# Kernel tuning notes

Measured on AMD Instinct MI355X. Metric: run time of the kernel, lower is better.

Reference implementation:

```python
import jax, jax.numpy as jnp
import numpy as np

DILATION_RATE = 4
SEGMENT_SIZE = 512


def setup_inputs() -> dict:
    key = jax.random.key(0)
    x = jax.random.normal(key, (4, 8192, 1024), dtype=jnp.float32)
    return {"x": x}


def reference(x):
    """LongNet-style dilated attention.

    For each offset in range(dilation_rate): take the strided slice
    x[:, offset::r, :], split it into segments of length `segment_size`,
    run full softmax(q k^T / sqrt(d)) v attention inside each segment
    (q=k=v=the slice; attention dim is the full d_model, matching how the
    original feeds [B, n_seg, seg, d_model] to FlashAttention), scatter the
    result back to the strided positions, and average the dilation heads
    (softmax over uniform logits == 1/r weights).

    Since seq_len % (r * segment_size) == 0, the r strided slices tile the
    sequence exactly, so we vectorize over offsets with a single reshape:
    position p = i*r + offset  ->  xr[:, i, offset, :].
    """
    r, seg = DILATION_RATE, SEGMENT_SIZE
    B, S, D = x.shape
    n = S // r            # tokens per strided slice
    g = n // seg          # segments per slice
    scale = 1.0 / jnp.sqrt(jnp.asarray(D, dtype=x.dtype))

    xs = x.reshape(B, g, seg, r, D)  # [B, g, seg, r, D]; axis r = dilation offset
    # segment-local attention, independently per (batch, offset, segment)
    scores = jnp.einsum("bgqrd,bgkrd->brgqk", xs, xs) * scale  # [B, r, g, seg, seg]
    probs = jax.nn.softmax(scores, axis=-1)
    out = jnp.einsum("brgqk,bgkrd->bgqrd", probs, xs)          # [B, g, seg, r, D]
    # scatter back to strided positions (pure reshape, since slices tile S),
    # then weighted sum with uniform softmax weights == divide by r.
    return out.reshape(B, S, D) / r
```

## Files before the change

kernel.cpp:

```cpp
#include <hip/hip_runtime.h>
#include <stdint.h>

typedef __bf16 bf16x8  __attribute__((ext_vector_type(8)));
typedef float  f32x4   __attribute__((ext_vector_type(4)));

#define LOG2E    1.44269504088896340736f
#define SM_SCALE 0.03125f

typedef __attribute__((address_space(1))) const uint32_t gau32;
typedef __attribute__((address_space(3))) uint32_t       lau32;
#define GLD16(g, l) __builtin_amdgcn_global_load_lds((gau32*)(g), (lau32*)(l), 16, 0, 0)

__device__ __forceinline__ uint32_t f2bf(float f) {
  uint32_t u = __builtin_bit_cast(uint32_t, f);
  u += 0x7FFFu + ((u >> 16) & 1u);
  return u >> 16;
}
__device__ __forceinline__ uint32_t pk2(float a, float b) {
  return f2bf(a) | (f2bf(b) << 16);
}
__device__ __forceinline__ uint4 pack8(float4 a, float4 b) {
  uint4 r;
  r.x = pk2(a.x, a.y); r.y = pk2(a.z, a.w);
  r.z = pk2(b.x, b.y); r.w = pk2(b.z, b.w);
  return r;
}

__global__ __launch_bounds__(256)
void prep_comb(const float* __restrict__ x, uint16_t* __restrict__ vt,
               uint16_t* __restrict__ xs) {
  __shared__ char tl[64 * 144];
  const int t    = threadIdx.x;
  const int blk  = blockIdx.x;
  const int dc   = blk & 15;
  const int kb   = (blk >> 4) & 7;
  const int prob = blk >> 7;
  const int b  = prob >> 4, off = (prob >> 2) & 3, gs = prob & 3;

  const int key = t >> 2, dq = t & 3;
  const float* src = x + ((size_t)(b * 8192 + gs * 2048 + (kb * 64 + key) * 4 + off)) * 1024
                     + dc * 64 + dq * 16;
  float4 f0 = *(const float4*)(src);
  float4 f1 = *(const float4*)(src + 4);
  float4 f2 = *(const float4*)(src + 8);
  float4 f3 = *(const float4*)(src + 12);
  const int swz = (key & 7) << 4;
  *(uint4*)(tl + key * 144 + ((dq * 32) ^ swz))      = pack8(f0, f1);
  *(uint4*)(tl + key * 144 + ((dq * 32 + 16) ^ swz)) = pack8(f2, f3);
  __syncthreads();
  {
    const int d = t >> 2, kq = t & 3;
    uint32_t w[8];
#pragma unroll
    for (int i = 0; i < 8; ++i) {
      int k0 = kq * 16 + 2 * i, k1 = k0 + 1;
      uint32_t a  = *(const uint16_t*)(tl + k0 * 144 + ((2 * d) ^ ((k0 & 7) << 4)));
      uint32_t bb = *(const uint16_t*)(tl + k1 * 144 + ((2 * d) ^ ((k1 & 7) << 4)));
      w[i] = a | (bb << 16);
    }
    uint16_t* dst = vt + ((size_t)(prob * 1024 + dc * 64 + d)) * 512 + kb * 64 + kq * 16;
    *(uint4*)(dst)     = *(uint4*)&w[0];
    *(uint4*)(dst + 8) = *(uint4*)&w[4];
  }
  {
    const int row = t >> 2, j = t & 3;
    uint4 w0 = *(const uint4*)(tl + row * 144 + j * 32);
    uint4 w1 = *(const uint4*)(tl + row * 144 + j * 32 + 16);
    char* dst = (char*)xs +
        ((size_t)((prob * 512 + kb * 64 + row) * 16 + dc)) * 128 + j * 32;
    *(uint4*)(dst)      = w0;
    *(uint4*)(dst + 16) = w1;
  }
}

#define B3_STRIDE 73728
#define B3_QOFF   65536
#define R3_0      65536
#define R3_1      67584
#define LDS3_BYTES 147456

__global__ __launch_bounds__(512, 2)
void dilattn3(const uint16_t* __restrict__ xs, const uint16_t* __restrict__ vt,
              float* __restrict__ out) {
  extern __shared__ char smem[];

  const int tid  = threadIdx.x;
  const int lane = tid & 63;
  const int wid  = tid >> 6;
  const int h    = lane >> 4;
  const int l15  = lane & 15;
  const int psw  = (l15 & 7) << 4;

  const int blk  = blockIdx.x;
  const int prob = ((blk & 7) << 3) | (blk >> 6);
  const int q0   = ((blk >> 3) & 7) * 64;
  const int b    = prob >> 4;
  const int off  = (prob >> 2) & 3;
  const int gs   = prob & 3;

  const char* xp = (const char*)xs + (size_t)prob * 1048576;

  const int r8 = lane >> 3, g8 = lane & 7;
  const char* gK = xp + (size_t)(wid * 8 + r8) * 2048 + g8 * 16;
  const char* gQ = xp + (size_t)(q0 + wid * 8 + r8) * 2048 + g8 * 16;

  const int akR = (64 * wid + l15) * 128;
  const int bqR = B3_QOFF + l15 * 128;
  const int fb0 = (16 * h) ^ psw;

  f32x4 S[4][4];
#pragma unroll
  for (int i = 0; i < 4; ++i)
#pragma unroll
    for (int j = 0; j < 4; ++j) S[i][j] = (f32x4){0.f, 0.f, 0.f, 0.f};

  {
    {
      char* base = smem;
#pragma unroll
      for (int ii = 0; ii < 8; ++ii)
        GLD16(gK + ii * 131072, base + wid * 1024 + ii * 8192);
      GLD16(gQ, base + B3_QOFF + wid * 1024);
    }
    __syncthreads();
#pragma unroll 1
    for (int dc = 0; dc < 16; ++dc) {
      if (dc < 15) {
        char* nb = smem + ((dc + 1) & 1) * B3_STRIDE;
        const int go = (dc + 1) * 128;
#pragma unroll
        for (int ii = 0; ii < 8; ++ii)
          GLD16(gK + ii * 131072 + go, nb + wid * 1024 + ii * 8192);
        GLD16(gQ + go, nb + B3_QOFF + wid * 1024);
      }
      const char* base = smem + (dc & 1) * B3_STRIDE;
#pragma unroll
      for (int s = 0; s < 2; ++s) {
        const int fb = fb0 ^ (s << 6);
        bf16x8 aK[4], bq[4];
#pragma unroll
        for (int kt = 0; kt < 4; ++kt)
          aK[kt] = *(const bf16x8*)(base + akR + kt * 2048 + fb);
#pragma unroll
        for (int qt = 0; qt < 4; ++qt)
          bq[qt] = *(const bf16x8*)(base + bqR + qt * 2048 + fb);
#pragma unroll
        for (int kt = 0; kt < 4; ++kt)
#pragma unroll
          for (int qt = 0; qt < 4; ++qt)
            S[kt][qt] = __builtin_amdgcn_mfma_f32_16x16x32_bf16(aK[kt], bq[qt], S[kt][qt], 0, 0, 0);
      }
      __syncthreads();
    }
  }

  float mq[4], sq[4], rinv[4];
#pragma unroll
  for (int qt = 0; qt < 4; ++qt) {
    float m = S[0][qt][0];
#pragma unroll
    for (int kt = 0; kt < 4; ++kt)
#pragma unroll
      for (int r = 0; r < 4; ++r) m = fmaxf(m, S[kt][qt][r]);
    m = fmaxf(m, __shfl_xor(m, 16, 64));
    m = fmaxf(m, __shfl_xor(m, 32, 64));
    mq[qt] = m;
  }
  if (h == 0) {
#pragma unroll
    for (int qt = 0; qt < 4; ++qt)
      *(float*)(smem + R3_0 + (wid * 64 + 16 * qt + l15) * 4) = mq[qt];
  }
  __syncthreads();
#pragma unroll
  for (int qt = 0; qt < 4; ++qt) {
    float m = -3e38f;
#pragma unroll
    for (int w = 0; w < 8; ++w)
      m = fmaxf(m, *(const float*)(smem + R3_0 + (w * 64 + 16 * qt + l15) * 4));
    mq[qt] = m * SM_SCALE;
    sq[qt] = 0.f;
  }
#pragma unroll
  for (int kt = 0; kt < 4; ++kt)
#pragma unroll
    for (int qt = 0; qt < 4; ++qt)
#pragma unroll
      for (int r = 0; r < 4; ++r) {
        float v = exp2f((S[kt][qt][r] * SM_SCALE - mq[qt]) * LOG2E);
        S[kt][qt][r] = v;
        sq[qt] += v;
      }
#pragma unroll
  for (int qt = 0; qt < 4; ++qt) {
    sq[qt] += __shfl_xor(sq[qt], 16, 64);
    sq[qt] += __shfl_xor(sq[qt], 32, 64);
  }
  if (h == 0) {
#pragma unroll
    for (int qt = 0; qt < 4; ++qt)
      *(float*)(smem + R3_1 + (wid * 64 + 16 * qt + l15) * 4) = sq[qt];
  }
  __syncthreads();
#pragma unroll
  for (int qt = 0; qt < 4; ++qt) {
    float l = 0.f;
#pragma unroll
    for (int w = 0; w < 8; ++w)
      l += *(const float*)(smem + R3_1 + (w * 64 + 16 * qt + l15) * 4);
    rinv[qt] = 0.25f / l;
  }
#pragma unroll
  for (int kt = 0; kt < 4; ++kt)
#pragma unroll
    for (int qt = 0; qt < 4; ++qt) {
      uint2 w2;
      w2.x = pk2(S[kt][qt][0] * rinv[qt], S[kt][qt][1] * rinv[qt]);
      w2.y = pk2(S[kt][qt][2] * rinv[qt], S[kt][qt][3] * rinv[qt]);
      *(uint2*)(smem + (16 * qt + l15) * 1024 +
                ((128 * wid + 32 * kt + 8 * h) ^ psw)) = w2;
    }
  __syncthreads();

  f32x4 acc[8][4];
#pragma unroll
  for (int i = 0; i < 8; ++i)
#pragma unroll
    for (int j = 0; j < 4; ++j) acc[i][j] = (f32x4){0.f, 0.f, 0.f, 0.f};

  const char* vtW = (const char*)(vt + ((size_t)(prob * 1024 + 128 * wid + l15)) * 512 + 8 * h);
  bf16x8 vcur[8], vnxt[8];
#pragma unroll
  for (int cd = 0; cd < 8; ++cd)
    vcur[cd] = *(const bf16x8*)(vtW + ((cd >> 2) * 64 + (cd & 3) * 16) * 1024);
#pragma unroll 1
  for (int ks = 0; ks < 16; ++ks) {
    if (ks < 15) {
#pragma unroll
      for (int cd = 0; cd < 8; ++cd)
        vnxt[cd] = *(const bf16x8*)(vtW + ((cd >> 2) * 64 + (cd & 3) * 16) * 1024 + (ks + 1) * 64);
    }
    bf16x8 pa[4];
#pragma unroll
    for (int qt = 0; qt < 4; ++qt)
      pa[qt] = *(const bf16x8*)(smem + (16 * qt + l15) * 1024 + ((64 * ks + 16 * h) ^ psw));
#pragma unroll
    for (int cd = 0; cd < 8; ++cd)
#pragma unroll
      for (int qt = 0; qt < 4; ++qt)
        acc[cd][qt] = __builtin_amdgcn_mfma_f32_16x16x32_bf16(pa[qt], vcur[cd], acc[cd][qt], 0, 0, 0);
#pragma unroll
    for (int cd = 0; cd < 8; ++cd) vcur[cd] = vnxt[cd];
  }

#pragma unroll
  for (int cd = 0; cd < 8; ++cd) {
    const int d = 128 * wid + (cd >> 2) * 64 + (cd & 3) * 16 + l15;
#pragma unroll
    for (int qt = 0; qt < 4; ++qt)
#pragma unroll
      for (int r = 0; r < 4; ++r) {
        const int qq = q0 + 16 * qt + 4 * h + r;
        out[((size_t)(b * 8192 + gs * 2048 + qq * 4 + off)) * 1024 + d] = acc[cd][qt][r];
      }
  }
}

#define KP_OFF 0
#define Q_OFF  65536
#define RED0   65536
#define RED1   67584
#define LDS_BYTES 73728

__global__ __launch_bounds__(256)
void vt_prepass(const float* __restrict__ x, uint16_t* __restrict__ vt) {
  __shared__ char tl[64 * 144];
  const int t    = threadIdx.x;
  const int blk  = blockIdx.x;
  const int dc   = blk & 15;
  const int kb   = (blk >> 4) & 7;
  const int prob = blk >> 7;
  const int b  = prob >> 4, off = (prob >> 2) & 3, gs = prob & 3;

  const int key = t >> 2, dq = t & 3;
  const float* src = x + ((size_t)(b * 8192 + gs * 2048 + (kb * 64 + key) * 4 + off)) * 1024
                     + dc * 64 + dq * 16;
  float4 f0 = *(const float4*)(src);
  float4 f1 = *(const float4*)(src + 4);
  float4 f2 = *(const float4*)(src + 8);
  float4 f3 = *(const float4*)(src + 12);
  const int swz = (key & 7) << 4;
  *(uint4*)(tl + key * 144 + ((dq * 32) ^ swz))      = pack8(f0, f1);
  *(uint4*)(tl + key * 144 + ((dq * 32 + 16) ^ swz)) = pack8(f2, f3);
  __syncthreads();
  const int d = t >> 2, kq = t & 3;
  uint32_t w[8];
#pragma unroll
  for (int i = 0; i < 8; ++i) {
    int k0 = kq * 16 + 2 * i, k1 = k0 + 1;
    uint32_t a  = *(const uint16_t*)(tl + k0 * 144 + ((2 * d) ^ ((k0 & 7) << 4)));
    uint32_t bb = *(const uint16_t*)(tl + k1 * 144 + ((2 * d) ^ ((k1 & 7) << 4)));
    w[i] = a | (bb << 16);
  }
  uint16_t* dst = vt + ((size_t)(prob * 1024 + dc * 64 + d)) * 512 + kb * 64 + kq * 16;
  *(uint4*)(dst)     = *(uint4*)&w[0];
  *(uint4*)(dst + 8) = *(uint4*)&w[4];
}

template <int USE_VT>
__global__ __launch_bounds__(512, 2)
void dilattn2(const float* __restrict__ x, const uint16_t* __restrict__ vt,
              float* __restrict__ out) {
  extern __shared__ char smem[];

  const int tid  = threadIdx.x;
  const int lane = tid & 63;
  const int wid  = tid >> 6;
  const int h    = lane >> 4;
  const int l15  = lane & 15;
  const int psw  = (l15 & 7) << 4;

  const int blk  = blockIdx.x;
  const int prob = blk >> 3;
  const int q0   = (blk & 7) * 64;
  const int b    = prob >> 4;
  const int off  = (prob >> 2) & 3;
  const int gs   = prob & 3;

  const float* xb = x + (size_t)b * (8192u * 1024u);

  const int srow = tid >> 3;
  const int sg   = tid & 7;
  const float* gK = xb + (size_t)(gs * 2048 + srow * 4 + off) * 1024 + sg * 8;
  const float* gQ = xb + (size_t)(gs * 2048 + (q0 + srow) * 4 + off) * 1024 + sg * 8;
  const int kWr = srow * 128 + ((sg * 16) ^ ((srow & 7) << 4));
  const int qWr = Q_OFF + kWr;

  const int akR = (64 * wid + l15) * 128;
  const int bqR = Q_OFF + l15 * 128;
  const int fb0 = (16 * h) ^ psw;

  f32x4 S[4][4];
#pragma unroll
  for (int i = 0; i < 4; ++i)
#pragma unroll
    for (int j = 0; j < 4; ++j) S[i][j] = (f32x4){0.f, 0.f, 0.f, 0.f};

  float4 kp[16], qp[2];
#pragma unroll
  for (int j = 0; j < 8; ++j) {
    const float* p = gK + (size_t)j * 262144;
    kp[2 * j]     = *(const float4*)(p);
    kp[2 * j + 1] = *(const float4*)(p + 4);
  }
  qp[0] = *(const float4*)(gQ);
  qp[1] = *(const float4*)(gQ + 4);

#pragma unroll 1
  for (int dc = 0; dc < 16; ++dc) {
#pragma unroll
    for (int j = 0; j < 8; ++j)
      *(uint4*)(smem + KP_OFF + kWr + j * 8192) = pack8(kp[2 * j], kp[2 * j + 1]);
    *(uint4*)(smem + qWr) = pack8(qp[0], qp[1]);
    if (dc < 15) {
      const int doff = (dc + 1) * 64;
#pragma unroll
      for (int j = 0; j < 8; ++j) {
        const float* p = gK + (size_t)j * 262144 + doff;
        kp[2 * j]     = *(const float4*)(p);
        kp[2 * j + 1] = *(const float4*)(p + 4);
      }
      qp[0] = *(const float4*)(gQ + doff);
      qp[1] = *(const float4*)(gQ + doff + 4);
    }
    __syncthreads();
#pragma unroll
    for (int s = 0; s < 2; ++s) {
      const int fb = fb0 ^ (s << 6);
      bf16x8 aK[4], bq[4];
#pragma unroll
      for (int kt = 0; kt < 4; ++kt)
        aK[kt] = *(const bf16x8*)(smem + akR + kt * 2048 + fb);
#pragma unroll
      for (int qt = 0; qt < 4; ++qt)
        bq[qt] = *(const bf16x8*)(smem + bqR + qt * 2048 + fb);
#pragma unroll
      for (int kt = 0; kt < 4; ++kt)
#pragma unroll
        for (int qt = 0; qt < 4; ++qt)
          S[kt][qt] = __builtin_amdgcn_mfma_f32_16x16x32_bf16(aK[kt], bq[qt], S[kt][qt], 0, 0, 0);
    }
    __syncthreads();
  }

  float mq[4], sq[4], rinv[4];
#pragma unroll
  for (int qt = 0; qt < 4; ++qt) {
    float m = S[0][qt][0];
#pragma unroll
    for (int kt = 0; kt < 4; ++kt)
#pragma unroll
      for (int r = 0; r < 4; ++r) m = fmaxf(m, S[kt][qt][r]);
    m = fmaxf(m, __shfl_xor(m, 16, 64));
    m = fmaxf(m, __shfl_xor(m, 32, 64));
    mq[qt] = m;
  }
  if (h == 0) {
#pragma unroll
    for (int qt = 0; qt < 4; ++qt)
      *(float*)(smem + RED0 + (wid * 64 + 16 * qt + l15) * 4) = mq[qt];
  }
  __syncthreads();
#pragma unroll
  for (int qt = 0; qt < 4; ++qt) {
    float m = -3e38f;
#pragma unroll
    for (int w = 0; w < 8; ++w)
      m = fmaxf(m, *(const float*)(smem + RED0 + (w * 64 + 16 * qt + l15) * 4));
    mq[qt] = m * SM_SCALE;
    sq[qt] = 0.f;
  }
#pragma unroll
  for (int kt = 0; kt < 4; ++kt)
#pragma unroll
    for (int qt = 0; qt < 4; ++qt)
#pragma unroll
      for (int r = 0; r < 4; ++r) {
        float v = exp2f((S[kt][qt][r] * SM_SCALE - mq[qt]) * LOG2E);
        S[kt][qt][r] = v;
        sq[qt] += v;
      }
#pragma unroll
  for (int qt = 0; qt < 4; ++qt) {
    sq[qt] += __shfl_xor(sq[qt], 16, 64);
    sq[qt] += __shfl_xor(sq[qt], 32, 64);
  }
  if (h == 0) {
#pragma unroll
    for (int qt = 0; qt < 4; ++qt)
      *(float*)(smem + RED1 + (wid * 64 + 16 * qt + l15) * 4) = sq[qt];
  }
  __syncthreads();
#pragma unroll
  for (int qt = 0; qt < 4; ++qt) {
    float l = 0.f;
#pragma unroll
    for (int w = 0; w < 8; ++w)
      l += *(const float*)(smem + RED1 + (w * 64 + 16 * qt + l15) * 4);
    rinv[qt] = 0.25f / l;
  }
#pragma unroll
  for (int kt = 0; kt < 4; ++kt)
#pragma unroll
    for (int qt = 0; qt < 4; ++qt) {
      uint2 w2;
      w2.x = pk2(S[kt][qt][0] * rinv[qt], S[kt][qt][1] * rinv[qt]);
      w2.y = pk2(S[kt][qt][2] * rinv[qt], S[kt][qt][3] * rinv[qt]);
      *(uint2*)(smem + KP_OFF + (16 * qt + l15) * 1024 +
                ((128 * wid + 32 * kt + 8 * h) ^ psw)) = w2;
    }
  __syncthreads();

  f32x4 acc[8][4];
#pragma unroll
  for (int i = 0; i < 8; ++i)
#pragma unroll
    for (int j = 0; j < 4; ++j) acc[i][j] = (f32x4){0.f, 0.f, 0.f, 0.f};

  const uint16_t* vtW = nullptr;
  if constexpr (USE_VT)
    vtW = vt + ((size_t)(prob * 1024 + 128 * wid + l15)) * 512 + 8 * h;

#pragma unroll 1
  for (int ks = 0; ks < 16; ++ks) {
    bf16x8 pa[4];
#pragma unroll
    for (int qt = 0; qt < 4; ++qt)
      pa[qt] = *(const bf16x8*)(smem + KP_OFF + (16 * qt + l15) * 1024 +
                                ((64 * ks + 16 * h) ^ psw));
#pragma unroll
    for (int cd = 0; cd < 8; ++cd) {
      bf16x8 v;
      if constexpr (USE_VT) {
        v = *(const bf16x8*)(vtW + (size_t)((cd >> 2) * 64 + (cd & 3) * 16) * 512 + 32 * ks);
      } else {
        const int d = 128 * wid + (cd >> 2) * 64 + (cd & 3) * 16 + l15;
        union { bf16x8 v; uint16_t u[8]; } a0;
#pragma unroll
        for (int jj = 0; jj < 8; ++jj) {
          int key = 32 * ks + 8 * h + jj;
          a0.u[jj] = (uint16_t)f2bf(xb[(size_t)(gs * 2048 + key * 4 + off) * 1024 + d]);
        }
        v = a0.v;
      }
#pragma unroll
      for (int qt = 0; qt < 4; ++qt)
        acc[cd][qt] = __builtin_amdgcn_mfma_f32_16x16x32_bf16(pa[qt], v, acc[cd][qt], 0, 0, 0);
    }
  }

#pragma unroll
  for (int cd = 0; cd < 8; ++cd) {
    const int d = 128 * wid + (cd >> 2) * 64 + (cd & 3) * 16 + l15;
#pragma unroll
    for (int qt = 0; qt < 4; ++qt)
#pragma unroll
      for (int r = 0; r < 4; ++r) {
        const int qq = q0 + 16 * qt + 4 * h + r;
        out[((size_t)(b * 8192 + gs * 2048 + qq * 4 + off)) * 1024 + d] = acc[cd][qt][r];
      }
  }
}

extern "C" void kernel_launch(void* const* d_in, const int* in_sizes, int n_in,
                              void* d_out, int out_size, void* d_ws, size_t ws_size,
                              hipStream_t stream) {
  const float* x = (const float*)d_in[0];
  float* out = (float*)d_out;
  (void)in_sizes; (void)n_in; (void)out_size;
  const size_t vt_bytes = 64ull * 1024 * 512 * 2;
  const size_t xs_bytes = 64ull * 512 * 16 * 128;
  if (ws_size >= vt_bytes + xs_bytes) {
    uint16_t* vtp = (uint16_t*)d_ws;
    uint16_t* xsp = (uint16_t*)((char*)d_ws + vt_bytes);
    hipFuncSetAttribute(reinterpret_cast<const void*>(dilattn3),
                        hipFuncAttributeMaxDynamicSharedMemorySize, LDS3_BYTES);
    prep_comb<<<8192, 256, 0, stream>>>(x, vtp, xsp);
    dilattn3<<<512, 512, LDS3_BYTES, stream>>>(xsp, vtp, out);
  } else if (ws_size >= vt_bytes) {
    uint16_t* vtp = (uint16_t*)d_ws;
    hipFuncSetAttribute(reinterpret_cast<const void*>(dilattn2<1>),
                        hipFuncAttributeMaxDynamicSharedMemorySize, LDS_BYTES);
    vt_prepass<<<8192, 256, 0, stream>>>(x, vtp);
    dilattn2<1><<<512, 512, LDS_BYTES, stream>>>(x, vtp, out);
  } else {
    hipFuncSetAttribute(reinterpret_cast<const void*>(dilattn2<0>),
                        hipFuncAttributeMaxDynamicSharedMemorySize, LDS_BYTES);
    dilattn2<0><<<512, 512, LDS_BYTES, stream>>>(x, nullptr, out);
  }
}
```

Before: 190.7 us.

## Restructure QK and PV loops with single barrier, prefetch V early, setprio MFMA

The QK^T loop now uses one barrier per iteration that waits only on vmcnt, so the global-to-LDS load for the next chunk is issued after that barrier instead of with a second sync. All LDS fragments are loaded before a prioritized MFMA burst. The first two V chunks are prefetched before the softmax phase, and the PV loop uses two ping-pong V register buffers so each load has a full MFMA block to hide its latency. Softmax barriers wait only on lgkmcnt. These changes raise register pressure and tighten the synchronization correctness margins.

```diff
diff --git a/kernel.cpp b/kernel.cpp
--- a/kernel.cpp
+++ b/kernel.cpp
@@ -10,6 +10,9 @@
 typedef __attribute__((address_space(1))) const uint32_t gau32;
 typedef __attribute__((address_space(3))) uint32_t       lau32;
 #define GLD16(g, l) __builtin_amdgcn_global_load_lds((gau32*)(g), (lau32*)(l), 16, 0, 0)
+
+#define LGKM_BAR() do { asm volatile("s_waitcnt lgkmcnt(0)" ::: "memory"); \
+  __builtin_amdgcn_s_barrier(); asm volatile("" ::: "memory"); } while (0)
 
 __device__ __forceinline__ uint32_t f2bf(float f) {
   uint32_t u = __builtin_bit_cast(uint32_t, f);
@@ -115,43 +118,55 @@
     for (int j = 0; j < 4; ++j) S[i][j] = (f32x4){0.f, 0.f, 0.f, 0.f};
 
   {
-    {
-      char* base = smem;
+    char* base0 = smem;
+#pragma unroll
+    for (int ii = 0; ii < 8; ++ii)
+      GLD16(gK + ii * 131072, base0 + wid * 1024 + ii * 8192);
+    GLD16(gQ, base0 + B3_QOFF + wid * 1024);
+  }
+#pragma unroll 1
+  for (int dc = 0; dc < 16; ++dc) {
+    asm volatile("s_waitcnt vmcnt(0)" ::: "memory");
+    __builtin_amdgcn_s_barrier();
+    asm volatile("" ::: "memory");
+    if (dc < 15) {
+      char* nb = smem + ((dc + 1) & 1) * B3_STRIDE;
+      const int go = (dc + 1) * 128;
 #pragma unroll
       for (int ii = 0; ii < 8; ++ii)
-        GLD16(gK + ii * 131072, base + wid * 1024 + ii * 8192);
-      GLD16(gQ, base + B3_QOFF + wid * 1024);
-    }
-    __syncthreads();
-#pragma unroll 1
-    for (int dc = 0; dc < 16; ++dc) {
-      if (dc < 15) {
-        char* nb = smem + ((dc + 1) & 1) * B3_STRIDE;
-        const int go = (dc + 1) * 128;
-#pragma unroll
-        for (int ii = 0; ii < 8; ++ii)
-          GLD16(gK + ii * 131072 + go, nb + wid * 1024 + ii * 8192);
-        GLD16(gQ + go, nb + B3_QOFF + wid * 1024);
-      }
-      const char* base = smem + (dc & 1) * B3_STRIDE;
-#pragma unroll
-      for (int s = 0; s < 2; ++s) {
-        const int fb = fb0 ^ (s << 6);
-        bf16x8 aK[4], bq[4];
-#pragma unroll
-        for (int kt = 0; kt < 4; ++kt)
-          aK[kt] = *(const bf16x8*)(base + akR + kt * 2048 + fb);
+        GLD16(gK + ii * 131072 + go, nb + wid * 1024 + ii * 8192);
+      GLD16(gQ + go, nb + B3_QOFF + wid * 1024);
+    }
+    const char* base = smem + (dc & 1) * B3_STRIDE;
+    bf16x8 aK[8], bq[8];
+#pragma unroll
+    for (int s = 0; s < 2; ++s) {
+      const int fb = fb0 ^ (s << 6);
+#pragma unroll
+      for (int kt = 0; kt < 4; ++kt)
+        aK[s * 4 + kt] = *(const bf16x8*)(base + akR + kt * 2048 + fb);
+#pragma unroll
+      for (int qt = 0; qt < 4; ++qt)
+        bq[s * 4 + qt] = *(const bf16x8*)(base + bqR + qt * 2048 + fb);
+    }
+    __builtin_amdgcn_s_setprio(1);
+#pragma unroll
+    for (int s = 0; s < 2; ++s)
+#pragma unroll
+      for (int kt = 0; kt < 4; ++kt)
 #pragma unroll
         for (int qt = 0; qt < 4; ++qt)
-          bq[qt] = *(const bf16x8*)(base + bqR + qt * 2048 + fb);
-#pragma unroll
-        for (int kt = 0; kt < 4; ++kt)
-#pragma unroll
-          for (int qt = 0; qt < 4; ++qt)
-            S[kt][qt] = __builtin_amdgcn_mfma_f32_16x16x32_bf16(aK[kt], bq[qt], S[kt][qt], 0, 0, 0);
-      }
-      __syncthreads();
-    }
+          S[kt][qt] = __builtin_amdgcn_mfma_f32_16x16x32_bf16(aK[s * 4 + kt], bq[s * 4 + qt],
+                                                              S[kt][qt], 0, 0, 0);
+    __builtin_amdgcn_s_setprio(0);
+  }
+
+  const char* vtW = (const char*)(vt + ((size_t)(prob * 1024 + 128 * wid + l15)) * 512 + 8 * h);
+  bf16x8 vA[8], vB[8];
+#pragma unroll
+  for (int cd = 0; cd < 8; ++cd) {
+    vA[cd] = *(const bf16x8*)(vtW + ((cd >> 2) * 64 + (cd & 3) * 16) * 1024);
+    vB[cd] = *(const bf16x8*)(vtW + ((cd >> 2) * 64 + (cd & 3) * 16) * 1024 + 64);
   }
 
   float mq[4], sq[4], rinv[4];
@@ -171,7 +186,7 @@
     for (int qt = 0; qt < 4; ++qt)
       *(float*)(smem + R3_0 + (wid * 64 + 16 * qt + l15) * 4) = mq[qt];
   }
-  __syncthreads();
+  LGKM_BAR();
 #pragma unroll
   for (int qt = 0; qt < 4; ++qt) {
     float m = -3e38f;
@@ -201,7 +216,7 @@
     for (int qt = 0; qt < 4; ++qt)
       *(float*)(smem + R3_1 + (wid * 64 + 16 * qt + l15) * 4) = sq[qt];
   }
-  __syncthreads();
+  LGKM_BAR();
 #pragma unroll
   for (int qt = 0; qt < 4; ++qt) {
     float l = 0.f;
@@ -220,7 +235,7 @@
       *(uint2*)(smem + (16 * qt + l15) * 1024 +
                 ((128 * wid + 32 * kt + 8 * h) ^ psw)) = w2;
     }
-  __syncthreads();
+  LGKM_BAR();
 
   f32x4 acc[8][4];
 #pragma unroll
@@ -228,29 +243,44 @@
 #pragma unroll
     for (int j = 0; j < 4; ++j) acc[i][j] = (f32x4){0.f, 0.f, 0.f, 0.f};
 
-  const char* vtW = (const char*)(vt + ((size_t)(prob * 1024 + 128 * wid + l15)) * 512 + 8 * h);
-  bf16x8 vcur[8], vnxt[8];
-#pragma unroll
-  for (int cd = 0; cd < 8; ++cd)
-    vcur[cd] = *(const bf16x8*)(vtW + ((cd >> 2) * 64 + (cd & 3) * 16) * 1024);
 #pragma unroll 1
-  for (int ks = 0; ks < 16; ++ks) {
-    if (ks < 15) {
+  for (int ks = 0; ks < 16; ks += 2) {
+    {
+      bf16x8 pa[4];
+#pragma unroll
+      for (int qt = 0; qt < 4; ++qt)
+        pa[qt] = *(const bf16x8*)(smem + (16 * qt + l15) * 1024 + ((64 * ks + 16 * h) ^ psw));
+      __builtin_amdgcn_s_setprio(1);
 #pragma unroll
       for (int cd = 0; cd < 8; ++cd)
-        vnxt[cd] = *(const bf16x8*)(vtW + ((cd >> 2) * 64 + (cd & 3) * 16) * 1024 + (ks + 1) * 64);
-    }
-    bf16x8 pa[4];
-#pragma unroll
-    for (int qt = 0; qt < 4; ++qt)
-      pa[qt] = *(const bf16x8*)(smem + (16 * qt + l15) * 1024 + ((64 * ks + 16 * h) ^ psw));
-#pragma unroll
-    for (int cd = 0; cd < 8; ++cd)
+#pragma unroll
+        for (int qt = 0; qt < 4; ++qt)
+          acc[cd][qt] = __builtin_amdgcn_mfma_f32_16x16x32_bf16(pa[qt], vA[cd], acc[cd][qt], 0, 0, 0);
+      __builtin_amdgcn_s_setprio(0);
+      if (ks + 2 < 16) {
+#pragma unroll
+        for (int cd = 0; cd < 8; ++cd)
+          vA[cd] = *(const bf16x8*)(vtW + ((cd >> 2) * 64 + (cd & 3) * 16) * 1024 + (ks + 2) * 64);
+      }
+    }
+    {
+      bf16x8 pa[4];
 #pragma unroll
       for (int qt = 0; qt < 4; ++qt)
-        acc[cd][qt] = __builtin_amdgcn_mfma_f32_16x16x32_bf16(pa[qt], vcur[cd], acc[cd][qt], 0, 0, 0);
-#pragma unroll
-    for (int cd = 0; cd < 8; ++cd) vcur[cd] = vnxt[cd];
+        pa[qt] = *(const bf16x8*)(smem + (16 * qt + l15) * 1024 + ((64 * (ks + 1) + 16 * h) ^ psw));
+      __builtin_amdgcn_s_setprio(1);
+#pragma unroll
+      for (int cd = 0; cd < 8; ++cd)
+#pragma unroll
+        for (int qt = 0; qt < 4; ++qt)
+          acc[cd][qt] = __builtin_amdgcn_mfma_f32_16x16x32_bf16(pa[qt], vB[cd], acc[cd][qt], 0, 0, 0);
+      __builtin_amdgcn_s_setprio(0);
+      if (ks + 3 < 16) {
+#pragma unroll
+        for (int cd = 0; cd < 8; ++cd)
+          vB[cd] = *(const bf16x8*)(vtW + ((cd >> 2) * 64 + (cd & 3) * 16) * 1024 + (ks + 3) * 64);
+      }
+    }
   }
 
 #pragma unroll
```

Result: faster. 182.7 us (-4.2%).

## Store X in MFMA fragment layout and stream K fragments directly from global

Applied to the files above, without the earlier changes.

The prep kernel now writes X in a per-16-row fragment-ordered layout so each lane loads its MFMA operand with a single contiguous 16-byte read. The attention kernel doubles to 16 waves (1024 threads), stages the full Q tile (all 1024 dims) in LDS once and reads K fragments straight from global into registers, which removes the double-buffered per-chunk LDS pipeline and its barriers. The PV stage also splits across 16 waves with fewer accumulators per wave. The trade-off is larger LDS use with a single block per CU, more cross-wave softmax reduction work, and no explicit prefetch of V.

```diff
diff --git a/kernel.cpp b/kernel.cpp
--- a/kernel.cpp
+++ b/kernel.cpp
@@ -28,7 +28,7 @@
 
 __global__ __launch_bounds__(256)
 void prep_comb(const float* __restrict__ x, uint16_t* __restrict__ vt,
-               uint16_t* __restrict__ xs) {
+               uint16_t* __restrict__ xf) {
   __shared__ char tl[64 * 144];
   const int t    = threadIdx.x;
   const int blk  = blockIdx.x;
@@ -63,24 +63,48 @@
     *(uint4*)(dst + 8) = *(uint4*)&w[4];
   }
   {
-    const int row = t >> 2, j = t & 3;
-    uint4 w0 = *(const uint4*)(tl + row * 144 + j * 32);
-    uint4 w1 = *(const uint4*)(tl + row * 144 + j * 32 + 16);
-    char* dst = (char*)xs +
-        ((size_t)((prob * 512 + kb * 64 + row) * 16 + dc)) * 128 + j * 32;
-    *(uint4*)(dst)      = w0;
-    *(uint4*)(dst + 16) = w1;
-  }
-}
-
-#define B3_STRIDE 73728
-#define B3_QOFF   65536
-#define R3_0      65536
-#define R3_1      67584
-#define LDS3_BYTES 147456
-
-__global__ __launch_bounds__(512, 2)
-void dilattn3(const uint16_t* __restrict__ xs, const uint16_t* __restrict__ vt,
+    const int row = t >> 2, p = t & 3;
+    const int dcl = p >> 1;
+    const int dq8b = (p & 1) * 2;
+    const int swz2 = (row & 7) << 4;
+    char* fbase = (char*)xf +
+        (((size_t)(prob * 32 + kb * 4 + (row >> 4)) * 32) + (dc * 2 + dcl)) * 1024;
+#pragma unroll
+    for (int i = 0; i < 2; ++i) {
+      const int dq8 = dq8b + i;
+      uint4 w = *(const uint4*)(tl + row * 144 + ((dcl * 64 + dq8 * 16) ^ swz2));
+      *(uint4*)(fbase + ((row & 15) + 16 * dq8) * 16) = w;
+    }
+  }
+}
+
+#define R4_0 131072
+#define R4_1 135168
+#define LDS4_BYTES 139264
+
+#define QKT_BODY(dc, A0, A1)                                                   \
+  {                                                                            \
+    const char* qb = smem + ((dc) >> 4) * 65536 + ((dc) & 15) * 4096 + lane16; \
+    bf16x8 b0 = *(const bf16x8*)(qb);                                          \
+    bf16x8 b1 = *(const bf16x8*)(qb + 1024);                                   \
+    bf16x8 b2 = *(const bf16x8*)(qb + 2048);                                   \
+    bf16x8 b3 = *(const bf16x8*)(qb + 3072);                                   \
+    S[0][0] = __builtin_amdgcn_mfma_f32_16x16x32_bf16(A0, b0, S[0][0], 0, 0, 0); \
+    S[0][1] = __builtin_amdgcn_mfma_f32_16x16x32_bf16(A0, b1, S[0][1], 0, 0, 0); \
+    S[0][2] = __builtin_amdgcn_mfma_f32_16x16x32_bf16(A0, b2, S[0][2], 0, 0, 0); \
+    S[0][3] = __builtin_amdgcn_mfma_f32_16x16x32_bf16(A0, b3, S[0][3], 0, 0, 0); \
+    S[1][0] = __builtin_amdgcn_mfma_f32_16x16x32_bf16(A1, b0, S[1][0], 0, 0, 0); \
+    S[1][1] = __builtin_amdgcn_mfma_f32_16x16x32_bf16(A1, b1, S[1][1], 0, 0, 0); \
+    S[1][2] = __builtin_amdgcn_mfma_f32_16x16x32_bf16(A1, b2, S[1][2], 0, 0, 0); \
+    S[1][3] = __builtin_amdgcn_mfma_f32_16x16x32_bf16(A1, b3, S[1][3], 0, 0, 0); \
+  }
+
+#define LOADA(dc, A0, A1) do {                       \
+    A0 = *(const bf16x8*)(xfA0 + (dc) * 1024);       \
+    A1 = *(const bf16x8*)(xfA1 + (dc) * 1024); } while (0)
+
+__global__ __launch_bounds__(1024, 4)
+void dilattn4(const char* __restrict__ xf, const char* __restrict__ vt,
               float* __restrict__ out) {
   extern __shared__ char smem[];
 
@@ -90,6 +114,7 @@
   const int h    = lane >> 4;
   const int l15  = lane & 15;
   const int psw  = (l15 & 7) << 4;
+  const int lane16 = lane * 16;
 
   const int blk  = blockIdx.x;
   const int prob = ((blk & 7) << 3) | (blk >> 6);
@@ -98,60 +123,39 @@
   const int off  = (prob >> 2) & 3;
   const int gs   = prob & 3;
 
-  const char* xp = (const char*)xs + (size_t)prob * 1048576;
-
-  const int r8 = lane >> 3, g8 = lane & 7;
-  const char* gK = xp + (size_t)(wid * 8 + r8) * 2048 + g8 * 16;
-  const char* gQ = xp + (size_t)(q0 + wid * 8 + r8) * 2048 + g8 * 16;
-
-  const int akR = (64 * wid + l15) * 128;
-  const int bqR = B3_QOFF + l15 * 128;
-  const int fb0 = (16 * h) ^ psw;
-
-  f32x4 S[4][4];
-#pragma unroll
-  for (int i = 0; i < 4; ++i)
+  const char* xfp = xf + (size_t)prob * 1048576;
+  const int qtile0 = q0 >> 4;
+
+#pragma unroll
+  for (int half = 0; half < 2; ++half)
+#pragma unroll
+    for (int i = 0; i < 4; ++i) {
+      const int c = wid * 4 + i;
+      const int dcl = c >> 2, qt = c & 3;
+      const char* src = xfp + ((size_t)(qtile0 + qt) * 32 + (half * 16 + dcl)) * 1024 + lane16;
+      GLD16(src, smem + half * 65536 + dcl * 4096 + qt * 1024);
+    }
+
+  const char* xfA0 = xfp + (size_t)(2 * wid) * 32768 + lane16;
+  const char* xfA1 = xfA0 + 32768;
+
+  f32x4 S[2][4];
+#pragma unroll
+  for (int i = 0; i < 2; ++i)
 #pragma unroll
     for (int j = 0; j < 4; ++j) S[i][j] = (f32x4){0.f, 0.f, 0.f, 0.f};
 
-  {
-    {
-      char* base = smem;
-#pragma unroll
-      for (int ii = 0; ii < 8; ++ii)
-        GLD16(gK + ii * 131072, base + wid * 1024 + ii * 8192);
-      GLD16(gQ, base + B3_QOFF + wid * 1024);
-    }
-    __syncthreads();
-#pragma unroll 1
-    for (int dc = 0; dc < 16; ++dc) {
-      if (dc < 15) {
-        char* nb = smem + ((dc + 1) & 1) * B3_STRIDE;
-        const int go = (dc + 1) * 128;
-#pragma unroll
-        for (int ii = 0; ii < 8; ++ii)
-          GLD16(gK + ii * 131072 + go, nb + wid * 1024 + ii * 8192);
-        GLD16(gQ + go, nb + B3_QOFF + wid * 1024);
-      }
-      const char* base = smem + (dc & 1) * B3_STRIDE;
-#pragma unroll
-      for (int s = 0; s < 2; ++s) {
-        const int fb = fb0 ^ (s << 6);
-        bf16x8 aK[4], bq[4];
-#pragma unroll
-        for (int kt = 0; kt < 4; ++kt)
-          aK[kt] = *(const bf16x8*)(base + akR + kt * 2048 + fb);
-#pragma unroll
-        for (int qt = 0; qt < 4; ++qt)
-          bq[qt] = *(const bf16x8*)(base + bqR + qt * 2048 + fb);
-#pragma unroll
-        for (int kt = 0; kt < 4; ++kt)
-#pragma unroll
-          for (int qt = 0; qt < 4; ++qt)
-            S[kt][qt] = __builtin_amdgcn_mfma_f32_16x16x32_bf16(aK[kt], bq[qt], S[kt][qt], 0, 0, 0);
-      }
-      __syncthreads();
-    }
+  bf16x8 aP0, aP1, aQ0, aQ1;
+  LOADA(0, aP0, aP1);
+  LOADA(1, aQ0, aQ1);
+  __syncthreads();
+
+#pragma unroll
+  for (int dc2 = 0; dc2 < 32; dc2 += 2) {
+    QKT_BODY(dc2, aP0, aP1);
+    if (dc2 + 2 < 32) LOADA(dc2 + 2, aP0, aP1);
+    QKT_BODY(dc2 + 1, aQ0, aQ1);
+    if (dc2 + 3 < 32) LOADA(dc2 + 3, aQ0, aQ1);
   }
 
   float mq[4], sq[4], rinv[4];
@@ -159,7 +163,7 @@
   for (int qt = 0; qt < 4; ++qt) {
     float m = S[0][qt][0];
 #pragma unroll
-    for (int kt = 0; kt < 4; ++kt)
+    for (int kt = 0; kt < 2; ++kt)
 #pragma unroll
       for (int r = 0; r < 4; ++r) m = fmaxf(m, S[kt][qt][r]);
     m = fmaxf(m, __shfl_xor(m, 16, 64));
@@ -169,20 +173,20 @@
   if (h == 0) {
 #pragma unroll
     for (int qt = 0; qt < 4; ++qt)
-      *(float*)(smem + R3_0 + (wid * 64 + 16 * qt + l15) * 4) = mq[qt];
+      *(float*)(smem + R4_0 + (wid * 64 + 16 * qt + l15) * 4) = mq[qt];
   }
   __syncthreads();
 #pragma unroll
   for (int qt = 0; qt < 4; ++qt) {
     float m = -3e38f;
 #pragma unroll
-    for (int w = 0; w < 8; ++w)
-      m = fmaxf(m, *(const float*)(smem + R3_0 + (w * 64 + 16 * qt + l15) * 4));
+    for (int w = 0; w < 16; ++w)
+      m = fmaxf(m, *(const float*)(smem + R4_0 + (w * 64 + 16 * qt + l15) * 4));
     mq[qt] = m * SM_SCALE;
     sq[qt] = 0.f;
   }
 #pragma unroll
-  for (int kt = 0; kt < 4; ++kt)
+  for (int kt = 0; kt < 2; ++kt)
 #pragma unroll
     for (int qt = 0; qt < 4; ++qt)
 #pragma unroll
@@ -199,71 +203,66 @@
   if (h == 0) {
 #pragma unroll
     for (int qt = 0; qt < 4; ++qt)
-      *(float*)(smem + R3_1 + (wid * 64 + 16 * qt + l15) * 4) = sq[qt];
+      *(float*)(smem + R4_1 + (wid * 64 + 16 * qt + l15) * 4) = sq[qt];
   }
   __syncthreads();
 #pragma unroll
   for (int qt = 0; qt < 4; ++qt) {
     float l = 0.f;
 #pragma unroll
-    for (int w = 0; w < 8; ++w)
-      l += *(const float*)(smem + R3_1 + (w * 64 + 16 * qt + l15) * 4);
+    for (int w = 0; w < 16; ++w)
+      l += *(const float*)(smem + R4_1 + (w * 64 + 16 * qt + l15) * 4);
     rinv[qt] = 0.25f / l;
   }
 #pragma unroll
-  for (int kt = 0; kt < 4; ++kt)
+  for (int kt = 0; kt < 2; ++kt)
 #pragma unroll
     for (int qt = 0; qt < 4; ++qt) {
       uint2 w2;
       w2.x = pk2(S[kt][qt][0] * rinv[qt], S[kt][qt][1] * rinv[qt]);
       w2.y = pk2(S[kt][qt][2] * rinv[qt], S[kt][qt][3] * rinv[qt]);
       *(uint2*)(smem + (16 * qt + l15) * 1024 +
-                ((128 * wid + 32 * kt + 8 * h) ^ psw)) = w2;
-    }
-  __syncthreads();
-
-  f32x4 acc[8][4];
-#pragma unroll
-  for (int i = 0; i < 8; ++i)
+                ((64 * wid + 32 * kt + 8 * h) ^ psw)) = w2;
+    }
+  __syncthreads();
+
+  f32x4 acc[4][4];
+#pragma unroll
+  for (int i = 0; i < 4; ++i)
 #pragma unroll
     for (int j = 0; j < 4; ++j) acc[i][j] = (f32x4){0.f, 0.f, 0.f, 0.f};
 
-  const char* vtW = (const char*)(vt + ((size_t)(prob * 1024 + 128 * wid + l15)) * 512 + 8 * h);
-  bf16x8 vcur[8], vnxt[8];
-#pragma unroll
-  for (int cd = 0; cd < 8; ++cd)
-    vcur[cd] = *(const bf16x8*)(vtW + ((cd >> 2) * 64 + (cd & 3) * 16) * 1024);
-#pragma unroll 1
+  const char* vtW = vt + (size_t)prob * 1048576 + (size_t)(64 * wid + l15) * 1024 + 16 * h;
+  const char* paB = smem + l15 * 1024;
+
+#pragma unroll 2
   for (int ks = 0; ks < 16; ++ks) {
-    if (ks < 15) {
-#pragma unroll
-      for (int cd = 0; cd < 8; ++cd)
-        vnxt[cd] = *(const bf16x8*)(vtW + ((cd >> 2) * 64 + (cd & 3) * 16) * 1024 + (ks + 1) * 64);
-    }
+    bf16x8 v0 = *(const bf16x8*)(vtW + 0 * 16384 + ks * 64);
+    bf16x8 v1 = *(const bf16x8*)(vtW + 1 * 16384 + ks * 64);
+    bf16x8 v2 = *(const bf16x8*)(vtW + 2 * 16384 + ks * 64);
+    bf16x8 v3 = *(const bf16x8*)(vtW + 3 * 16384 + ks * 64);
     bf16x8 pa[4];
 #pragma unroll
     for (int qt = 0; qt < 4; ++qt)
-      pa[qt] = *(const bf16x8*)(smem + (16 * qt + l15) * 1024 + ((64 * ks + 16 * h) ^ psw));
-#pragma unroll
-    for (int cd = 0; cd < 8; ++cd)
-#pragma unroll
-      for (int qt = 0; qt < 4; ++qt)
-        acc[cd][qt] = __builtin_amdgcn_mfma_f32_16x16x32_bf16(pa[qt], vcur[cd], acc[cd][qt], 0, 0, 0);
-#pragma unroll
-    for (int cd = 0; cd < 8; ++cd) vcur[cd] = vnxt[cd];
-  }
-
-#pragma unroll
-  for (int cd = 0; cd < 8; ++cd) {
-    const int d = 128 * wid + (cd >> 2) * 64 + (cd & 3) * 16 + l15;
-#pragma unroll
-    for (int qt = 0; qt < 4; ++qt)
-#pragma unroll
-      for (int r = 0; r < 4; ++r) {
-        const int qq = q0 + 16 * qt + 4 * h + r;
-        out[((size_t)(b * 8192 + gs * 2048 + qq * 4 + off)) * 1024 + d] = acc[cd][qt][r];
-      }
-  }
+      pa[qt] = *(const bf16x8*)(paB + qt * 16384 + ((64 * ks + 16 * h) ^ psw));
+#pragma unroll
+    for (int qt = 0; qt < 4; ++qt) {
+      acc[0][qt] = __builtin_amdgcn_mfma_f32_16x16x32_bf16(pa[qt], v0, acc[0][qt], 0, 0, 0);
+      acc[1][qt] = __builtin_amdgcn_mfma_f32_16x16x32_bf16(pa[qt], v1, acc[1][qt], 0, 0, 0);
+      acc[2][qt] = __builtin_amdgcn_mfma_f32_16x16x32_bf16(pa[qt], v2, acc[2][qt], 0, 0, 0);
+      acc[3][qt] = __builtin_amdgcn_mfma_f32_16x16x32_bf16(pa[qt], v3, acc[3][qt], 0, 0, 0);
+    }
+  }
+
+  float* outW = out + ((size_t)(b * 8192 + gs * 2048 + (q0 + 4 * h) * 4 + off)) * 1024
+                + 64 * wid + l15;
+#pragma unroll
+  for (int cd = 0; cd < 4; ++cd)
+#pragma unroll
+    for (int qt = 0; qt < 4; ++qt)
+#pragma unroll
+      for (int r = 0; r < 4; ++r)
+        outW[(size_t)((16 * qt + r) * 4) * 1024 + cd * 16] = acc[cd][qt][r];
 }
 
 #define KP_OFF 0
@@ -519,14 +518,14 @@
   float* out = (float*)d_out;
   (void)in_sizes; (void)n_in; (void)out_size;
   const size_t vt_bytes = 64ull * 1024 * 512 * 2;
-  const size_t xs_bytes = 64ull * 512 * 16 * 128;
-  if (ws_size >= vt_bytes + xs_bytes) {
+  const size_t xf_bytes = 64ull * 1024 * 1024;
+  if (ws_size >= vt_bytes + xf_bytes) {
     uint16_t* vtp = (uint16_t*)d_ws;
-    uint16_t* xsp = (uint16_t*)((char*)d_ws + vt_bytes);
-    hipFuncSetAttribute(reinterpret_cast<const void*>(dilattn3),
-                        hipFuncAttributeMaxDynamicSharedMemorySize, LDS3_BYTES);
-    prep_comb<<<8192, 256, 0, stream>>>(x, vtp, xsp);
-    dilattn3<<<512, 512, LDS3_BYTES, stream>>>(xsp, vtp, out);
+    uint16_t* xfp = (uint16_t*)((char*)d_ws + vt_bytes);
+    hipFuncSetAttribute(reinterpret_cast<const void*>(dilattn4),
+                        hipFuncAttributeMaxDynamicSharedMemorySize, LDS4_BYTES);
+    prep_comb<<<8192, 256, 0, stream>>>(x, vtp, xfp);
+    dilattn4<<<512, 1024, LDS4_BYTES, stream>>>((const char*)xfp, (const char*)vtp, out);
   } else if (ws_size >= vt_bytes) {
     uint16_t* vtp = (uint16_t*)d_ws;
     hipFuncSetAttribute(reinterpret_cast<const void*>(dilattn2<1>),
```

Measured after the change: 185.0 us. -3.0%, faster.
